# Kernel optimization log

Measured on AMD Instinct MI355X. Metric: run time of the kernel, lower is better.

Reference implementation:

```python
import jax, jax.numpy as jnp
import numpy as np

B, N, E, H = 2, 2048, 1024, 16
HD = E // H  # head_dim = 64


def setup_inputs() -> dict:
    key = jax.random.key(0)
    k1, k2, k3, k4, k5 = jax.random.split(key, 5)
    x = jax.random.normal(k1, (B, N, E), dtype=jnp.float32)
    # per-head Linear(E, 3*HD): stacked weights [H, E, 3*HD] and biases [H, 3*HD]
    Wqkv = jax.random.normal(k2, (H, E, 3 * HD), dtype=jnp.float32) * (1.0 / np.sqrt(E))
    bqkv = jax.random.normal(k3, (H, 3 * HD), dtype=jnp.float32) * 0.01
    Wout = jax.random.normal(k4, (E, E), dtype=jnp.float32) * (1.0 / np.sqrt(E))
    bout = jax.random.normal(k5, (E,), dtype=jnp.float32) * 0.01
    return {"x": x, "Wqkv": Wqkv, "bqkv": bqkv, "Wout": Wout, "bout": bout}


def reference(x, Wqkv, bqkv, Wout, bout):
    # per-head QKV projection, vectorized over heads: [B, H, N, 3*HD]
    proj = jnp.einsum('bne,hef->bhnf', x, Wqkv) + bqkv[None, :, None, :]
    k, q, v = jnp.split(proj, 3, axis=-1)  # each [B, H, N, HD]
    # scores = q @ k^T / sqrt(HD): [B, H, N, N]
    scores = jnp.einsum('bhqd,bhkd->bhqk', q, k) / jnp.sqrt(jnp.asarray(HD, dtype=x.dtype))
    # causal mask (tril)
    causal = jnp.tril(jnp.ones((N, N), dtype=bool))
    scores = jnp.where(causal[None, None, :, :], scores, -jnp.inf)
    attn = jax.nn.softmax(scores, axis=-1)
    sa = jnp.einsum('bhqk,bhkd->bhqd', attn, v)  # [B, H, N, HD]
    # concat heads in order -> [B, N, E]
    sa = jnp.transpose(sa, (0, 2, 1, 3)).reshape(B, N, E)
    return sa @ Wout + bout
```

## Files before the change

### kernel.cpp

```cpp
#include <hip/hip_runtime.h>
#include <hip/hip_bf16.h>

#define Bz 2
#define Nn 2048
#define Ee 1024
#define Hh 16
#define HD 64

typedef unsigned short u16;
typedef unsigned int u32;

typedef __bf16 bf16x8 __attribute__((ext_vector_type(8)));
typedef float f32x4 __attribute__((ext_vector_type(4)));

__device__ __forceinline__ float bf2f(u16 u) {
    u32 v = ((u32)u) << 16;
    return __builtin_bit_cast(float, v);
}
__device__ __forceinline__ u16 f2bf(float f) {
    u32 i = __builtin_bit_cast(u32, f);
    u32 r = (i + 0x7FFFu + ((i >> 16) & 1u)) >> 16;
    return (u16)r;
}
__device__ __forceinline__ u32 pack2(float a, float b) {
    return (u32)f2bf(a) | ((u32)f2bf(b) << 16);
}
__device__ __forceinline__ bf16x8 ld_frag(const u16* p) {
    return __builtin_bit_cast(bf16x8, *(const uint4*)p);
}
__device__ __forceinline__ f32x4 zero4() {
    f32x4 z; z[0]=0.f; z[1]=0.f; z[2]=0.f; z[3]=0.f; return z;
}

__device__ __forceinline__ void async_copy16(const u16* g, u16* l) {
    __builtin_amdgcn_global_load_lds(
        (const __attribute__((address_space(1))) u32*)g,
        (__attribute__((address_space(3))) u32*)l, 16, 0, 0);
}

__global__ void ws_diag(float* out, float code) { out[0] = code; }

__global__ __launch_bounds__(256) void convert_x(
    const float* __restrict__ x, u16* __restrict__ xbf)
{
    size_t idx = ((size_t)blockIdx.x * 256 + threadIdx.x) * 8;
    float4 f0 = *(const float4*)(x + idx);
    float4 f1 = *(const float4*)(x + idx + 4);
    uint4 pk;
    pk.x = pack2(f0.x, f0.y); pk.y = pack2(f0.z, f0.w);
    pk.z = pack2(f1.x, f1.y); pk.w = pack2(f1.z, f1.w);
    *(uint4*)(xbf + idx) = pk;
}

__global__ __launch_bounds__(256) void transpose_f32_bf16(
    const float* __restrict__ src, u16* __restrict__ dst, int R, int C)
{
    const int r0 = blockIdx.x * 64, c0 = blockIdx.y * 64;
    const size_t zoff = (size_t)blockIdx.z * R * C;
    src += zoff; dst += zoff;
    const int tid = threadIdx.x;

    __shared__ float T[64][65];
    {
        int tr = tid >> 2, tc = (tid & 3) * 16;
        const float* s = src + (size_t)(r0 + tr) * C + c0 + tc;
#pragma unroll
        for (int j = 0; j < 4; ++j) {
            float4 v = ((const float4*)s)[j];
            T[tr][tc + 4 * j + 0] = v.x; T[tr][tc + 4 * j + 1] = v.y;
            T[tr][tc + 4 * j + 2] = v.z; T[tr][tc + 4 * j + 3] = v.w;
        }
    }
    __syncthreads();
    {
        int cc = tid >> 2, rr = (tid & 3) * 16;
        u16* d = dst + (size_t)(c0 + cc) * R + r0 + rr;
        u32 w[8];
#pragma unroll
        for (int i = 0; i < 8; ++i)
            w[i] = pack2(T[rr + 2 * i][cc], T[rr + 2 * i + 1][cc]);
        *(uint4*)(d)     = make_uint4(w[0], w[1], w[2], w[3]);
        *(uint4*)(d + 8) = make_uint4(w[4], w[5], w[6], w[7]);
    }
}

__global__ __launch_bounds__(256) void transpose_v(
    const u16* __restrict__ src, u16* __restrict__ dst)
{
    const int n0 = blockIdx.x * 64;
    const size_t z = blockIdx.y;
    src += z * (size_t)Nn * HD;
    dst += z * (size_t)HD * Nn;
    const int tid = threadIdx.x;

    __shared__ u16 T[64][66];
    {
        int tr = tid >> 2, tc = (tid & 3) * 16;
        const u16* s = src + (size_t)(n0 + tr) * HD + tc;
        *(uint4*)&T[tr][tc]     = *(const uint4*)(s);
        *(uint4*)&T[tr][tc + 8] = *(const uint4*)(s + 8);
    }
    __syncthreads();
    {
        int cc = tid >> 2, rr = (tid & 3) * 16;
        u32 w[8];
#pragma unroll
        for (int i = 0; i < 8; ++i)
            w[i] = (u32)T[rr + 2 * i][cc] | ((u32)T[rr + 2 * i + 1][cc] << 16);
        u16* d = dst + (size_t)cc * Nn + n0 + rr;
        *(uint4*)(d)     = make_uint4(w[0], w[1], w[2], w[3]);
        *(uint4*)(d + 8) = make_uint4(w[4], w[5], w[6], w[7]);
    }
}

__global__ __launch_bounds__(256) void qkv_mfma(
    const u16* __restrict__ xbf, const u16* __restrict__ Wt,
    const float* __restrict__ bias,
    u16* __restrict__ kbuf, u16* __restrict__ qbuf, u16* __restrict__ vbuf)
{
    const int mt = blockIdx.x;
    const int h  = blockIdx.y;
    const int tid = threadIdx.x;
    const int lane = tid & 63, wid = tid >> 6;
    const int quad = lane >> 4, l15 = lane & 15;

    __shared__ u16 As[64 * 64];
    __shared__ u16 Bs[192 * 64];

    f32x4 acc[4][3];
#pragma unroll
    for (int mi = 0; mi < 4; ++mi)
#pragma unroll
        for (int ni = 0; ni < 3; ++ni) acc[mi][ni] = zero4();

    const u16* xb = xbf + (size_t)mt * 64 * Ee;
    const u16* wtb = Wt + (size_t)h * 192 * 1024;

    const int arowl = lane >> 3;
    const int jj = (lane & 7) ^ arowl;

    for (int kb = 0; kb < 16; ++kb) {
        __syncthreads();
#pragma unroll
        for (int i = 0; i < 2; ++i) {
            int rbase = (wid * 2 + i) * 8;
            const u16* g = xb + (size_t)(rbase + arowl) * Ee + kb * 64 + jj * 8;
            async_copy16(g, &As[(wid * 2 + i) * 512]);
        }
#pragma unroll
        for (int i = 0; i < 6; ++i) {
            int rbase = (wid * 6 + i) * 8;
            const u16* g = wtb + (size_t)(rbase + arowl) * 1024 + kb * 64 + jj * 8;
            async_copy16(g, &Bs[(wid * 6 + i) * 512]);
        }
        __syncthreads();

#pragma unroll
        for (int kk0 = 0; kk0 < 2; ++kk0) {
            const int pos = ((kk0 * 4 + quad) ^ (l15 & 7)) * 8;
            bf16x8 af[4], bf[3];
#pragma unroll
            for (int mi = 0; mi < 4; ++mi)
                af[mi] = ld_frag(&As[(mi * 16 + l15) * 64 + pos]);
#pragma unroll
            for (int ni = 0; ni < 3; ++ni)
                bf[ni] = ld_frag(&Bs[(wid * 48 + ni * 16 + l15) * 64 + pos]);
#pragma unroll
            for (int mi = 0; mi < 4; ++mi)
#pragma unroll
                for (int ni = 0; ni < 3; ++ni)
                    acc[mi][ni] = __builtin_amdgcn_mfma_f32_16x16x32_bf16(
                        af[mi], bf[ni], acc[mi][ni], 0, 0, 0);
        }
    }

#pragma unroll
    for (int ni = 0; ni < 3; ++ni) {
        int col = wid * 48 + ni * 16 + l15;
        int ft = col >> 6, d = col & 63;
        u16* dst = (ft == 0) ? kbuf : (ft == 1) ? qbuf : vbuf;
        float bv = bias[h * 192 + col];
#pragma unroll
        for (int mi = 0; mi < 4; ++mi)
#pragma unroll
            for (int r = 0; r < 4; ++r) {
                int gm = mt * 64 + mi * 16 + quad * 4 + r;
                int bb = gm >> 11, n = gm & (Nn - 1);
                dst[(((size_t)(bb * Hh + h)) * Nn + n) * HD + d] =
                    f2bf(acc[mi][ni][r] + bv);
            }
    }
}

__global__ __launch_bounds__(256) void attn2(
    const u16* __restrict__ qbuf, const u16* __restrict__ kbuf,
    const u16* __restrict__ vtb, u16* __restrict__ p0buf,
    u16* __restrict__ p1buf, float* __restrict__ ml)
{
    const int id = blockIdx.x;
    const int bh = (id & 7) * 4 + ((id >> 3) & 3);
    const int p  = id >> 5;
    const int tid = threadIdx.x;
    const int lane = tid & 63, wid = tid >> 6;
    const int l15 = lane & 15, quad = lane >> 4;

    __shared__ u16 KsL[2][4096];
    __shared__ u16 VtL[2][4096];

    const u16* qb = qbuf + (size_t)bh * Nn * HD;
    const u16* kb = kbuf + (size_t)bh * Nn * HD;
    const u16* vt = vtb + (size_t)bh * HD * Nn;

    const int r_l = lane >> 3;
    const int jj = (lane & 7) ^ r_l;
    const int xsw = l15 & 7;
    const int src0 = l15 + (quad & 1) * 32;
    const bool qhi = quad >= 2;
    const float SC = 0.18033688f;

    for (int sg = 0; sg < 2; ++sg) {
        const int qt = sg ? (31 - p) : p;
        const int T  = qt + 1;
        const int t0 = sg ? ((T + 1) >> 1) : 0;
        const int t1 = sg ? T : ((p + 2) >> 1);
        u16*   pb = sg ? p1buf : p0buf;
        float* mb = ml + (sg ? 131072 : 0);
        float* lb = ml + (sg ? 196608 : 65536);

        const int qrow = qt * 64 + wid * 16 + l15;

        f32x4 oacc[4];
#pragma unroll
        for (int dt = 0; dt < 4; ++dt) oacc[dt] = zero4();
        float m_i = -3e38f, l_i = 0.f;

        if (t0 < t1) {
            bf16x8 qf[2];
#pragma unroll
            for (int st = 0; st < 2; ++st)
                qf[st] = __builtin_bit_cast(bf16x8,
                    *(const uint4*)(qb + (size_t)qrow * HD + st * 32 + quad * 8));

            __syncthreads();
#pragma unroll
            for (int i2 = 0; i2 < 4; ++i2) {
                int idx = wid * 4 + i2;
                if (idx < 8) {
                    const u16* g = kb + (size_t)(t0 * 64 + idx * 8 + r_l) * HD + jj * 8;
                    async_copy16(g, &KsL[0][idx * 512]);
                } else {
                    int ii = idx - 8;
                    const u16* g = vt + (size_t)(ii * 8 + r_l) * Nn + t0 * 64 + jj * 8;
                    async_copy16(g, &VtL[0][ii * 512]);
                }
            }

            const int nit = t1 - t0;
            for (int i = 0; i < nit; ++i) {
                const int tk = t0 + i;
                __syncthreads();
                if (i + 1 < nit) {
                    const int nb = (i + 1) & 1;
#pragma unroll
                    for (int i2 = 0; i2 < 4; ++i2) {
                        int idx = wid * 4 + i2;
                        if (idx < 8) {
                            const u16* g = kb + (size_t)((tk + 1) * 64 + idx * 8 + r_l) * HD + jj * 8;
                            async_copy16(g, &KsL[nb][idx * 512]);
                        } else {
                            int ii = idx - 8;
                            const u16* g = vt + (size_t)(ii * 8 + r_l) * Nn + (tk + 1) * 64 + jj * 8;
                            async_copy16(g, &VtL[nb][ii * 512]);
                        }
                    }
                }
                const u16* K = KsL[i & 1];
                const u16* V = VtL[i & 1];

                f32x4 s[4];
#pragma unroll
                for (int t = 0; t < 4; ++t) {
                    f32x4 a = zero4();
#pragma unroll
                    for (int st = 0; st < 2; ++st) {
                        bf16x8 kf = ld_frag(&K[(t * 16 + l15) * 64 +
                                               ((st * 4 + quad) ^ xsw) * 8]);
                        a = __builtin_amdgcn_mfma_f32_16x16x32_bf16(kf, qf[st], a, 0, 0, 0);
                    }
                    s[t] = a;
                }

                if (tk == qt) {
#pragma unroll
                    for (int t = 0; t < 4; ++t)
#pragma unroll
                        for (int r = 0; r < 4; ++r) {
                            int key = tk * 64 + t * 16 + quad * 4 + r;
                            float v = s[t][r] * SC;
                            if (key > qrow) v = -3e38f;
                            s[t][r] = v;
                        }
                } else {
#pragma unroll
                    for (int t = 0; t < 4; ++t)
#pragma unroll
                        for (int r = 0; r < 4; ++r) s[t][r] *= SC;
                }

                float mx = s[0][0];
#pragma unroll
                for (int t = 0; t < 4; ++t)
#pragma unroll
                    for (int r = 0; r < 4; ++r) mx = fmaxf(mx, s[t][r]);
                mx = fmaxf(mx, __shfl_xor(mx, 16));
                mx = fmaxf(mx, __shfl_xor(mx, 32));
                float mn = fmaxf(m_i, mx);
                float alpha = exp2f(m_i - mn);
                m_i = mn;
                float rs = 0.f;
#pragma unroll
                for (int t = 0; t < 4; ++t)
#pragma unroll
                    for (int r = 0; r < 4; ++r) {
                        float e = exp2f(s[t][r] - mn);
                        s[t][r] = e;
                        rs += e;
                    }
                rs += __shfl_xor(rs, 16);
                rs += __shfl_xor(rs, 32);
                l_i = l_i * alpha + rs;
#pragma unroll
                for (int dt = 0; dt < 4; ++dt)
#pragma unroll
                    for (int r = 0; r < 4; ++r) oacc[dt][r] *= alpha;

                u32 pk[4][2];
#pragma unroll
                for (int t = 0; t < 4; ++t) {
                    pk[t][0] = pack2(s[t][0], s[t][1]);
                    pk[t][1] = pack2(s[t][2], s[t][3]);
                }
#pragma unroll
                for (int st = 0; st < 2; ++st) {
                    u32 e0 = pk[2 * st][0],     e1 = pk[2 * st][1];
                    u32 o0 = pk[2 * st + 1][0], o1 = pk[2 * st + 1][1];
                    u32 A0 = __shfl(e0, src0),      B0 = __shfl(o0, src0);
                    u32 A1 = __shfl(e1, src0),      B1 = __shfl(o1, src0);
                    u32 A2 = __shfl(e0, src0 + 16), B2 = __shfl(o0, src0 + 16);
                    u32 A3 = __shfl(e1, src0 + 16), B3 = __shfl(o1, src0 + 16);
                    u32 U0 = qhi ? B0 : A0;
                    u32 U1 = qhi ? B1 : A1;
                    u32 U2 = qhi ? B2 : A2;
                    u32 U3 = qhi ? B3 : A3;
                    bf16x8 pf = __builtin_bit_cast(bf16x8, make_uint4(U0, U1, U2, U3));
#pragma unroll
                    for (int dt = 0; dt < 4; ++dt) {
                        bf16x8 vf = ld_frag(&V[(dt * 16 + l15) * 64 +
                                               ((st * 4 + quad) ^ xsw) * 8]);
                        oacc[dt] = __builtin_amdgcn_mfma_f32_16x16x32_bf16(
                            vf, pf, oacc[dt], 0, 0, 0);
                    }
                }
            }
        }

#pragma unroll
        for (int dt = 0; dt < 4; ++dt) {
            ushort4 ov;
            ov.x = f2bf(oacc[dt][0]);
            ov.y = f2bf(oacc[dt][1]);
            ov.z = f2bf(oacc[dt][2]);
            ov.w = f2bf(oacc[dt][3]);
            *(ushort4*)&pb[((size_t)bh * Nn + qrow) * HD + dt * 16 + quad * 4] = ov;
        }
        if (quad == 0) {
            mb[bh * Nn + qrow] = m_i;
            lb[bh * Nn + qrow] = l_i;
        }
    }
}

__global__ __launch_bounds__(256) void attn_merge(
    const u16* __restrict__ p0, u16* __restrict__ p1,
    const float* __restrict__ ml)
{
    const int idx = blockIdx.x * 256 + threadIdx.x;
    const int row = idx >> 3;
    const int dc = (idx & 7) * 8;

    const float m1 = ml[row],          l1 = ml[65536 + row];
    const float m2 = ml[131072 + row], l2 = ml[196608 + row];
    const float m = fmaxf(m1, m2);
    const float a1 = exp2f(m1 - m), a2 = exp2f(m2 - m);
    const float inv = 1.f / (a1 * l1 + a2 * l2);
    const float s1 = a1 * inv, s2 = a2 * inv;

    const size_t off = (size_t)row * HD + dc;
    uint4 v0 = *(const uint4*)&p0[off];
    uint4 v1 = *(const uint4*)&p1[off];
    u32 a[4] = {v0.x, v0.y, v0.z, v0.w};
    u32 b[4] = {v1.x, v1.y, v1.z, v1.w};
    u32 w[4];
#pragma unroll
    for (int j = 0; j < 4; ++j) {
        float x0 = bf2f((u16)a[j]) * s1 + bf2f((u16)b[j]) * s2;
        float x1 = bf2f((u16)(a[j] >> 16)) * s1 + bf2f((u16)(b[j] >> 16)) * s2;
        w[j] = pack2(x0, x1);
    }
    *(uint4*)&p1[off] = make_uint4(w[0], w[1], w[2], w[3]);
}

typedef float f32x16 __attribute__((ext_vector_type(16)));
__device__ __forceinline__ f32x16 zero16() {
    f32x16 z;
#pragma unroll
    for (int i = 0; i < 16; ++i) z[i] = 0.f;
    return z;
}

__global__ __launch_bounds__(256) void out_mfma(
    const u16* __restrict__ A, const u16* __restrict__ Wt,
    const float* __restrict__ bias, float* __restrict__ out)
{
    const int mt = blockIdx.x;
    const int nt = blockIdx.y;
    const int tid = threadIdx.x;
    const int lane = tid & 63, wid = tid >> 6;
    const int l31 = lane & 31, khalf = (lane >> 5) * 8;

    __shared__ u16 As[128][72];
    __shared__ u16 Bs[64][72];

    f32x16 acc[2];
    acc[0] = zero16(); acc[1] = zero16();

    const int arow = tid >> 1, akh = (tid & 1) * 32;
    const int gm = mt * 128 + arow;
    const int bb = gm >> 11, n = gm & (Nn - 1);
    const int brow = tid >> 2, bc = (tid & 3) * 16;

    for (int k0 = 0; k0 < Ee; k0 += 64) {
        __syncthreads();
        {
            const int c = k0 + akh;
            const int h = c >> 6, d0 = c & 63;
            const u16* asrc = A + (((size_t)(bb * Hh + h) * Nn + n) * HD + d0);
#pragma unroll
            for (int j = 0; j < 4; ++j)
                *(uint4*)&As[arow][akh + 8 * j] = *(const uint4*)(asrc + 8 * j);
            const u16* bsrc = Wt + (size_t)(nt * 64 + brow) * 1024 + k0 + bc;
            *(uint4*)&Bs[brow][bc]     = *(const uint4*)(bsrc);
            *(uint4*)&Bs[brow][bc + 8] = *(const uint4*)(bsrc + 8);
        }
        __syncthreads();
#pragma unroll
        for (int kc = 0; kc < 4; ++kc) {
            bf16x8 af = ld_frag(&As[wid * 32 + l31][kc * 16 + khalf]);
#pragma unroll
            for (int ct = 0; ct < 2; ++ct) {
                bf16x8 bf = ld_frag(&Bs[ct * 32 + l31][kc * 16 + khalf]);
                acc[ct] = __builtin_amdgcn_mfma_f32_32x32x16_bf16(af, bf, acc[ct], 0, 0, 0);
            }
        }
    }

#pragma unroll
    for (int ct = 0; ct < 2; ++ct) {
        int col = nt * 64 + ct * 32 + l31;
        float bv = bias[col];
#pragma unroll
        for (int r = 0; r < 16; ++r) {
            int row_l = (r & 3) + 8 * (r >> 2) + 4 * (lane >> 5);
            int gm2 = mt * 128 + wid * 32 + row_l;
            out[(size_t)gm2 * Ee + col] = acc[ct][r] + bv;
        }
    }
}

extern "C" void kernel_launch(void* const* d_in, const int* in_sizes, int n_in,
                              void* d_out, int out_size, void* d_ws, size_t ws_size,
                              hipStream_t stream) {
    const float* x    = (const float*)d_in[0];
    const float* Wqkv = (const float*)d_in[1];
    const float* bqkv = (const float*)d_in[2];
    const float* Wout = (const float*)d_in[3];
    const float* bout = (const float*)d_in[4];
    float* out = (float*)d_out;

    const size_t SZ = (size_t)Bz * Hh * Nn * HD;
    const size_t NSA = (size_t)Bz * Nn * Ee;
    const size_t NEED = (3 * SZ + NSA) * sizeof(u16);

    if (ws_size < NEED) {
        ws_diag<<<1, 1, 0, stream>>>(out, 20000.0f + (float)(ws_size >> 20));
        return;
    }

    u16* ws = (u16*)d_ws;
    u16* kbuf  = ws;
    u16* qbuf  = ws + SZ;
    u16* vbuf  = ws + 2 * SZ;
    u16* sabuf = ws + 3 * SZ;
    u16* wqkv_t = sabuf;
    u16* wout_t = kbuf;
    u16* xbf    = (u16*)d_out;
    u16* vtb    = (u16*)d_out + SZ;
    u16* p0     = (u16*)d_out;
    u16* p1     = vbuf;
    float* ml   = (float*)sabuf;

    convert_x<<<2048, 256, 0, stream>>>(x, xbf);
    transpose_f32_bf16<<<dim3(16, 3, 16), 256, 0, stream>>>(Wqkv, wqkv_t, 1024, 192);
    qkv_mfma<<<dim3(64, 16), 256, 0, stream>>>(xbf, wqkv_t, bqkv, kbuf, qbuf, vbuf);
    transpose_v<<<dim3(32, 32), 256, 0, stream>>>(vbuf, vtb);
    attn2<<<dim3(1024), 256, 0, stream>>>(qbuf, kbuf, vtb, p0, p1, ml);
    attn_merge<<<dim3(2048), 256, 0, stream>>>(p0, p1, ml);
    transpose_f32_bf16<<<dim3(16, 16, 1), 256, 0, stream>>>(Wout, wout_t, 1024, 1024);
    out_mfma<<<dim3(32, 16), 256, 0, stream>>>(p1, wout_t, bout, out);
}
```

Baseline: 205.4 us.

## Enlarge QKV GEMM tile, fold softmax scale into Q, cheaper bf16 pack

The QKV projection kernel now computes 128x192 tiles per block with a 2x2 warp layout, halving the grid. The goal is more reuse of each loaded weight tile and fewer blocks. The softmax scale is folded into Q when it is written out, removing per-score multiplies in the attention loop. P is packed to bf16 with round-half-up instead of round-to-nearest-even, which cuts ALU work at a small rounding difference. The larger tile raises accumulator register use and leaves fewer blocks to spread across the CUs.

```diff
diff --git a/kernel.cpp b/kernel.cpp
--- a/kernel.cpp
+++ b/kernel.cpp
@@ -13,6 +13,8 @@
 typedef __bf16 bf16x8 __attribute__((ext_vector_type(8)));
 typedef float f32x4 __attribute__((ext_vector_type(4)));
 
+#define QK_SCALE 0.18033688f
+
 __device__ __forceinline__ float bf2f(u16 u) {
     u32 v = ((u32)u) << 16;
     return __builtin_bit_cast(float, v);
@@ -24,6 +26,11 @@
 }
 __device__ __forceinline__ u32 pack2(float a, float b) {
     return (u32)f2bf(a) | ((u32)f2bf(b) << 16);
+}
+__device__ __forceinline__ u32 pack2h(float a, float b) {
+    u32 ua = __builtin_bit_cast(u32, a) + 0x8000u;
+    u32 ub = __builtin_bit_cast(u32, b) + 0x8000u;
+    return (ua >> 16) | (ub & 0xFFFF0000u);
 }
 __device__ __forceinline__ bf16x8 ld_frag(const u16* p) {
     return __builtin_bit_cast(bf16x8, *(const uint4*)p);
@@ -122,18 +129,19 @@
     const int h  = blockIdx.y;
     const int tid = threadIdx.x;
     const int lane = tid & 63, wid = tid >> 6;
+    const int wy = wid >> 1, wx = wid & 1;
     const int quad = lane >> 4, l15 = lane & 15;
 
-    __shared__ u16 As[64 * 64];
+    __shared__ u16 As[128 * 64];
     __shared__ u16 Bs[192 * 64];
 
-    f32x4 acc[4][3];
+    f32x4 acc[4][6];
 #pragma unroll
     for (int mi = 0; mi < 4; ++mi)
 #pragma unroll
-        for (int ni = 0; ni < 3; ++ni) acc[mi][ni] = zero4();
-
-    const u16* xb = xbf + (size_t)mt * 64 * Ee;
+        for (int ni = 0; ni < 6; ++ni) acc[mi][ni] = zero4();
+
+    const u16* xb = xbf + (size_t)mt * 128 * Ee;
     const u16* wtb = Wt + (size_t)h * 192 * 1024;
 
     const int arowl = lane >> 3;
@@ -142,10 +150,10 @@
     for (int kb = 0; kb < 16; ++kb) {
         __syncthreads();
 #pragma unroll
-        for (int i = 0; i < 2; ++i) {
-            int rbase = (wid * 2 + i) * 8;
+        for (int i = 0; i < 4; ++i) {
+            int rbase = (wid * 4 + i) * 8;
             const u16* g = xb + (size_t)(rbase + arowl) * Ee + kb * 64 + jj * 8;
-            async_copy16(g, &As[(wid * 2 + i) * 512]);
+            async_copy16(g, &As[(wid * 4 + i) * 512]);
         }
 #pragma unroll
         for (int i = 0; i < 6; ++i) {
@@ -158,36 +166,37 @@
 #pragma unroll
         for (int kk0 = 0; kk0 < 2; ++kk0) {
             const int pos = ((kk0 * 4 + quad) ^ (l15 & 7)) * 8;
-            bf16x8 af[4], bf[3];
+            bf16x8 af[4], bf[6];
 #pragma unroll
             for (int mi = 0; mi < 4; ++mi)
-                af[mi] = ld_frag(&As[(mi * 16 + l15) * 64 + pos]);
-#pragma unroll
-            for (int ni = 0; ni < 3; ++ni)
-                bf[ni] = ld_frag(&Bs[(wid * 48 + ni * 16 + l15) * 64 + pos]);
+                af[mi] = ld_frag(&As[(wy * 64 + mi * 16 + l15) * 64 + pos]);
+#pragma unroll
+            for (int ni = 0; ni < 6; ++ni)
+                bf[ni] = ld_frag(&Bs[(wx * 96 + ni * 16 + l15) * 64 + pos]);
 #pragma unroll
             for (int mi = 0; mi < 4; ++mi)
 #pragma unroll
-                for (int ni = 0; ni < 3; ++ni)
+                for (int ni = 0; ni < 6; ++ni)
                     acc[mi][ni] = __builtin_amdgcn_mfma_f32_16x16x32_bf16(
                         af[mi], bf[ni], acc[mi][ni], 0, 0, 0);
         }
     }
 
 #pragma unroll
-    for (int ni = 0; ni < 3; ++ni) {
-        int col = wid * 48 + ni * 16 + l15;
+    for (int ni = 0; ni < 6; ++ni) {
+        int col = wx * 96 + ni * 16 + l15;
         int ft = col >> 6, d = col & 63;
         u16* dst = (ft == 0) ? kbuf : (ft == 1) ? qbuf : vbuf;
+        float sc = (ft == 1) ? QK_SCALE : 1.0f;
         float bv = bias[h * 192 + col];
 #pragma unroll
         for (int mi = 0; mi < 4; ++mi)
 #pragma unroll
             for (int r = 0; r < 4; ++r) {
-                int gm = mt * 64 + mi * 16 + quad * 4 + r;
+                int gm = mt * 128 + wy * 64 + mi * 16 + quad * 4 + r;
                 int bb = gm >> 11, n = gm & (Nn - 1);
                 dst[(((size_t)(bb * Hh + h)) * Nn + n) * HD + d] =
-                    f2bf(acc[mi][ni][r] + bv);
+                    f2bf((acc[mi][ni][r] + bv) * sc);
             }
     }
 }
@@ -216,7 +225,6 @@
     const int xsw = l15 & 7;
     const int src0 = l15 + (quad & 1) * 32;
     const bool qhi = quad >= 2;
-    const float SC = 0.18033688f;
 
     for (int sg = 0; sg < 2; ++sg) {
         const int qt = sg ? (31 - p) : p;
@@ -296,15 +304,8 @@
 #pragma unroll
                         for (int r = 0; r < 4; ++r) {
                             int key = tk * 64 + t * 16 + quad * 4 + r;
-                            float v = s[t][r] * SC;
-                            if (key > qrow) v = -3e38f;
-                            s[t][r] = v;
+                            if (key > qrow) s[t][r] = -3e38f;
                         }
-                } else {
-#pragma unroll
-                    for (int t = 0; t < 4; ++t)
-#pragma unroll
-                        for (int r = 0; r < 4; ++r) s[t][r] *= SC;
                 }
 
                 float mx = s[0][0];
@@ -337,8 +338,8 @@
                 u32 pk[4][2];
 #pragma unroll
                 for (int t = 0; t < 4; ++t) {
-                    pk[t][0] = pack2(s[t][0], s[t][1]);
-                    pk[t][1] = pack2(s[t][2], s[t][3]);
+                    pk[t][0] = pack2h(s[t][0], s[t][1]);
+                    pk[t][1] = pack2h(s[t][2], s[t][3]);
                 }
 #pragma unroll
                 for (int st = 0; st < 2; ++st) {
@@ -511,7 +512,7 @@
 
     convert_x<<<2048, 256, 0, stream>>>(x, xbf);
     transpose_f32_bf16<<<dim3(16, 3, 16), 256, 0, stream>>>(Wqkv, wqkv_t, 1024, 192);
-    qkv_mfma<<<dim3(64, 16), 256, 0, stream>>>(xbf, wqkv_t, bqkv, kbuf, qbuf, vbuf);
+    qkv_mfma<<<dim3(32, 16), 256, 0, stream>>>(xbf, wqkv_t, bqkv, kbuf, qbuf, vbuf);
     transpose_v<<<dim3(32, 32), 256, 0, stream>>>(vbuf, vtb);
     attn2<<<dim3(1024), 256, 0, stream>>>(qbuf, kbuf, vtb, p0, p1, ml);
     attn_merge<<<dim3(2048), 256, 0, stream>>>(p0, p1, ml);
```

Result: faster. 196.9 us (-4.1%).
